# Kernel optimization log

Hardware: AMD Instinct MI355X
Metric: run time of the kernel (lower is better)

The kernel has to match this reference:

```python
import jax, jax.numpy as jnp
import numpy as np

N_NODES = 50000
N_EDGES = 600000
D = 128
BN_EPS = 1e-5


def _linear_init(key, fan_in, fan_out):
    # torch nn.Linear default: U(-1/sqrt(fan_in), 1/sqrt(fan_in)) for W and b
    kw, kb = jax.random.split(key)
    bound = 1.0 / np.sqrt(fan_in)
    W = jax.random.uniform(kw, (fan_in, fan_out), minval=-bound, maxval=bound, dtype=jnp.float32)
    b = jax.random.uniform(kb, (fan_out,), minval=-bound, maxval=bound, dtype=jnp.float32)
    return W, b


def setup_inputs() -> dict:
    key = jax.random.key(0)
    ks = jax.random.split(key, 8)
    x = jax.random.normal(ks[0], (N_NODES, D), dtype=jnp.float32)
    edge_index = jax.random.randint(ks[1], (2, N_EDGES), 0, N_NODES, dtype=jnp.int32)
    edge_attr = jax.random.normal(ks[2], (N_EDGES, D), dtype=jnp.float32)
    # MLP: [2D, D, D, D] -> Linear(2D,D)+SiLU+BN, Linear(D,D)+SiLU+BN, Linear(D,D)
    W1, b1 = _linear_init(ks[3], 2 * D, D)
    W2, b2 = _linear_init(ks[4], D, D)
    W3, b3 = _linear_init(ks[5], D, D)
    g1 = jnp.ones((D,), jnp.float32); be1 = jnp.zeros((D,), jnp.float32)
    g2 = jnp.ones((D,), jnp.float32); be2 = jnp.zeros((D,), jnp.float32)
    return {"x": x, "edge_index": edge_index, "edge_attr": edge_attr,
            "W1": W1, "b1": b1, "g1": g1, "be1": be1,
            "W2": W2, "b2": b2, "g2": g2, "be2": be2,
            "W3": W3, "b3": b3}


def _bn(h, gamma, beta):
    # BatchNorm1d in training mode: normalize with batch statistics (biased var)
    mean = jnp.mean(h, axis=0)
    var = jnp.var(h, axis=0)
    return (h - mean) * jax.lax.rsqrt(var + BN_EPS) * gamma + beta


def reference(x, edge_index, edge_attr, W1, b1, g1, be1, W2, b2, g2, be2, W3, b3):
    src = edge_index[0]
    # scatter_add over edges indexed by source node -> [N_NODES, D]
    agg = jax.ops.segment_sum(edge_attr, src, num_segments=x.shape[0])
    h = jnp.concatenate([x, agg], axis=1)  # [N, 2D]
    h = _bn(jax.nn.silu(h @ W1 + b1), g1, be1)
    h = _bn(jax.nn.silu(h @ W2 + b2), g2, be2)
    return h @ W3 + b3
```

## Files before the change

### kernel.cpp

```cpp
#include <hip/hip_runtime.h>
#include <hip/hip_bf16.h>

#define D 128

typedef __attribute__((ext_vector_type(8))) short bfrag;
typedef __attribute__((ext_vector_type(4))) float facc;
typedef __attribute__((ext_vector_type(4))) unsigned int u32x4;
typedef __attribute__((ext_vector_type(4))) float f32x4;

__device__ __forceinline__ facc mfma16(bfrag a, bfrag b, facc c) {
    return __builtin_amdgcn_mfma_f32_16x16x32_bf16(a, b, c, 0, 0, 0);
}
__device__ __forceinline__ unsigned int bf16_rn(float f) {
    unsigned int u = __float_as_uint(f);
    u += 0x7FFF + ((u >> 16) & 1);
    return u >> 16;
}
__device__ __forceinline__ float bf16_f(unsigned int h) {
    return __uint_as_float(h << 16);
}
__device__ __forceinline__ unsigned int packf(float v) {
    unsigned int hi = bf16_rn(v);
    unsigned int lo = bf16_rn(v - bf16_f(hi));
    return (hi << 16) | lo;
}

__global__ __launch_bounds__(256) void hist_kernel(
    const int* __restrict__ src, int* __restrict__ counts, int nedges) {
    int e = blockIdx.x * 256 + threadIdx.x;
    if (e < nedges) atomicAdd(&counts[src[e]], 1);
}

#define SCHUNK 2048
__global__ __launch_bounds__(256) void scanF_kernel(
    const int* __restrict__ counts, int* __restrict__ bsum,
    int* __restrict__ ctr, int* __restrict__ off, int* __restrict__ cur,
    int n, int nbk) {
    __shared__ int sd[256];
    __shared__ int sbase;
    const int tid = threadIdx.x;
    const int b = blockIdx.x;
    const int base = b * SCHUNK + tid * 8;
    int loc[8];
    int s = 0;
#pragma unroll
    for (int j = 0; j < 8; ++j) {
        int idx = base + j;
        int c = (idx < n) ? counts[idx] : 0;
        loc[j] = c;
        s += c;
    }
    sd[tid] = s;
    __syncthreads();
#pragma unroll
    for (int d2 = 1; d2 < 256; d2 <<= 1) {
        int t = (tid >= d2) ? sd[tid - d2] : 0;
        __syncthreads();
        sd[tid] += t;
        __syncthreads();
    }
    if (tid == 0) {
        atomicExch(&bsum[b], sd[255]);
        __threadfence();
        atomicAdd(ctr, 1);
        while (atomicAdd(ctr, 0) < nbk) __builtin_amdgcn_s_sleep(8);
    }
    __syncthreads();
    if (tid < 64) {
        int t = (tid < b) ? atomicAdd(&bsum[tid], 0) : 0;
#pragma unroll
        for (int o = 32; o; o >>= 1) t += __shfl_down(t, o);
        if (tid == 0) sbase = t;
    }
    __syncthreads();
    int pre = sbase + sd[tid] - s;
#pragma unroll
    for (int j = 0; j < 8; ++j) {
        int idx = base + j;
        if (idx < n) {
            off[idx] = pre;
            cur[idx] = pre;
            pre += loc[j];
        }
    }
    if (b == nbk - 1 && tid == 0) off[n] = sbase + sd[255];
}

__global__ void fill_kernel(const int* __restrict__ src, int* __restrict__ cur,
                            int* __restrict__ eid, int nedges) {
    int e = blockIdx.x * 256 + threadIdx.x;
    if (e < nedges) {
        int slot = atomicAdd(&cur[src[e]], 1);
        eid[slot] = e;
    }
}

__global__ __launch_bounds__(256) void gather_split_kernel(
    const float* __restrict__ edge_attr, const int* __restrict__ eid,
    const int* __restrict__ off, unsigned int* __restrict__ aggp, int nnodes,
    const float* __restrict__ x, unsigned int* __restrict__ xp, int n4,
    const float* __restrict__ W1, unsigned short* __restrict__ Wh,
    unsigned short* __restrict__ Wl, int gblk, int sblk) {
    const int b = blockIdx.x;
    if (b < gblk) {
        int node = b * 8 + (threadIdx.x >> 5);
        if (node >= nnodes) return;
        const int c = threadIdx.x & 31;
        int i = off[node];
        const int e = off[node + 1];
        f32x4 acc = {0.f, 0.f, 0.f, 0.f};

        for (; i + 8 <= e; i += 8) {
            int r0 = eid[i + 0], r1 = eid[i + 1], r2 = eid[i + 2],
                r3 = eid[i + 3], r4 = eid[i + 4], r5 = eid[i + 5],
                r6 = eid[i + 6], r7 = eid[i + 7];
            f32x4 v0 = __builtin_nontemporal_load(
                (const f32x4*)(edge_attr + (size_t)r0 * D) + c);
            f32x4 v1 = __builtin_nontemporal_load(
                (const f32x4*)(edge_attr + (size_t)r1 * D) + c);
            f32x4 v2 = __builtin_nontemporal_load(
                (const f32x4*)(edge_attr + (size_t)r2 * D) + c);
            f32x4 v3 = __builtin_nontemporal_load(
                (const f32x4*)(edge_attr + (size_t)r3 * D) + c);
            f32x4 v4 = __builtin_nontemporal_load(
                (const f32x4*)(edge_attr + (size_t)r4 * D) + c);
            f32x4 v5 = __builtin_nontemporal_load(
                (const f32x4*)(edge_attr + (size_t)r5 * D) + c);
            f32x4 v6 = __builtin_nontemporal_load(
                (const f32x4*)(edge_attr + (size_t)r6 * D) + c);
            f32x4 v7 = __builtin_nontemporal_load(
                (const f32x4*)(edge_attr + (size_t)r7 * D) + c);
            acc += (v0 + v1) + (v2 + v3) + ((v4 + v5) + (v6 + v7));
        }
        if (i + 4 <= e) {
            int r0 = eid[i + 0], r1 = eid[i + 1], r2 = eid[i + 2],
                r3 = eid[i + 3];
            f32x4 v0 = __builtin_nontemporal_load(
                (const f32x4*)(edge_attr + (size_t)r0 * D) + c);
            f32x4 v1 = __builtin_nontemporal_load(
                (const f32x4*)(edge_attr + (size_t)r1 * D) + c);
            f32x4 v2 = __builtin_nontemporal_load(
                (const f32x4*)(edge_attr + (size_t)r2 * D) + c);
            f32x4 v3 = __builtin_nontemporal_load(
                (const f32x4*)(edge_attr + (size_t)r3 * D) + c);
            acc += (v0 + v1) + (v2 + v3);
            i += 4;
        }
        if (i + 2 <= e) {
            int r0 = eid[i + 0], r1 = eid[i + 1];
            f32x4 v0 = __builtin_nontemporal_load(
                (const f32x4*)(edge_attr + (size_t)r0 * D) + c);
            f32x4 v1 = __builtin_nontemporal_load(
                (const f32x4*)(edge_attr + (size_t)r1 * D) + c);
            acc += v0 + v1;
            i += 2;
        }
        if (i < e) {
            acc += __builtin_nontemporal_load(
                (const f32x4*)(edge_attr + (size_t)eid[i] * D) + c);
        }
        u32x4 p;
#pragma unroll
        for (int r = 0; r < 4; ++r) p[r] = packf(acc[r]);
        *((u32x4*)(aggp + (size_t)node * D) + c) = p;
    } else if (b < gblk + sblk) {
        int i = (b - gblk) * 256 + threadIdx.x;
        if (i < n4) {
            float4 v = ((const float4*)x)[i];
            uint4 p;
            p.x = packf(v.x);
            p.y = packf(v.y);
            p.z = packf(v.z);
            p.w = packf(v.w);
            ((uint4*)xp)[i] = p;
        }
    } else {
        int j = b - gblk - sblk;
        int k = threadIdx.x;
        float w = W1[(size_t)k * D + j];
        unsigned int hi = bf16_rn(w);
        size_t o = (size_t)((k >> 3) * 128 + j) * 8 + (k & 7);
        Wh[o] = (unsigned short)hi;
        Wl[o] = (unsigned short)bf16_rn(w - bf16_f(hi));
    }
}

__global__ void fold_kernel(const float* __restrict__ sum,
                            const float* __restrict__ sq,
                            const float* __restrict__ gamma,
                            const float* __restrict__ beta,
                            const float* __restrict__ W,
                            const float* __restrict__ b,
                            unsigned short* __restrict__ Wh,
                            unsigned short* __restrict__ Wl,
                            float* __restrict__ bf, float invM) {
    int j = blockIdx.x;
    int k = threadIdx.x;
    float mean = sum[k] * invM;
    float var = sq[k] * invM - mean * mean;
    float scale = gamma[k] * rsqrtf(var + 1e-5f);
    float shift = beta[k] - mean * scale;
    float w = W[k * D + j];
    float wf = scale * w;
    unsigned int hi = bf16_rn(wf);
    size_t o = (size_t)((k >> 3) * 128 + j) * 8 + (k & 7);
    Wh[o] = (unsigned short)hi;
    Wl[o] = (unsigned short)bf16_rn(wf - bf16_f(hi));
    float v = shift * w;
#pragma unroll
    for (int of = 32; of; of >>= 1) v += __shfl_down(v, of);
    __shared__ float ws2[2];
    if ((k & 63) == 0) ws2[k >> 6] = v;
    __syncthreads();
    if (k == 0) bf[j] = b[j] + ws2[0] + ws2[1];
}

template <int K, bool SILU, bool STATS, bool PACKOUT>
__global__ __launch_bounds__(256, 2) void gemm_mfma(
    const unsigned int* __restrict__ A0, const unsigned int* __restrict__ A1,
    const unsigned short* __restrict__ Wh,
    const unsigned short* __restrict__ Wl,
    const float* __restrict__ bias, unsigned int* __restrict__ Cp,
    float* __restrict__ Cf, float* __restrict__ gsum,
    float* __restrict__ gsq, int M) {
    constexpr int NS = K / 32;
    const int tid = threadIdx.x;
    const int w = tid >> 6;
    const int l = tid & 63;
    const int lr = l & 15;
    const int lk = l >> 4;
    const int row0 = blockIdx.x * 128 + w * 32;

    facc acc[2][8];
#pragma unroll
    for (int rt = 0; rt < 2; ++rt)
#pragma unroll
        for (int ct = 0; ct < 8; ++ct)
#pragma unroll
            for (int r = 0; r < 4; ++r) acc[rt][ct][r] = 0.f;

    for (int s = 0; s < NS; ++s) {
        const int kb = s * 32 + lk * 8;
        bfrag ah[2], al[2];
#pragma unroll
        for (int rt = 0; rt < 2; ++rt) {
            const int arow = row0 + rt * 16 + lr;
            const unsigned int* As = A0;
            int kk = kb;
            if (K == 256 && s >= 4) { As = A1; kk = kb - 128; }
            u32x4 q0 = {0u, 0u, 0u, 0u}, q1 = {0u, 0u, 0u, 0u};
            if (arow < M) {
                const u32x4* p = (const u32x4*)(As + (size_t)arow * D + kk);
                q0 = p[0];
                q1 = p[1];
            }
            unsigned int ua[8] = {q0.x, q0.y, q0.z, q0.w,
                                  q1.x, q1.y, q1.z, q1.w};
            u32x4 uh, ul;
#pragma unroll
            for (int r = 0; r < 4; ++r) {
                uh[r] = __builtin_amdgcn_perm(ua[2 * r + 1], ua[2 * r],
                                              0x07060302u);
                ul[r] = __builtin_amdgcn_perm(ua[2 * r + 1], ua[2 * r],
                                              0x05040100u);
            }
            ah[rt] = __builtin_bit_cast(bfrag, uh);
            al[rt] = __builtin_bit_cast(bfrag, ul);
        }
        bfrag bh[8], bl[8];
        const int fb = (s * 4 + lk) * 128;
#pragma unroll
        for (int ct = 0; ct < 8; ++ct) {
            size_t o = (size_t)(fb + ct * 16 + lr) * 8;
            bh[ct] = *(const bfrag*)(Wh + o);
            bl[ct] = *(const bfrag*)(Wl + o);
        }
#pragma unroll
        for (int rt = 0; rt < 2; ++rt)
#pragma unroll
            for (int ct = 0; ct < 8; ++ct)
                acc[rt][ct] = mfma16(ah[rt], bh[ct], acc[rt][ct]);
#pragma unroll
        for (int rt = 0; rt < 2; ++rt)
#pragma unroll
            for (int ct = 0; ct < 8; ++ct)
                acc[rt][ct] = mfma16(ah[rt], bl[ct], acc[rt][ct]);
#pragma unroll
        for (int rt = 0; rt < 2; ++rt)
#pragma unroll
            for (int ct = 0; ct < 8; ++ct)
                acc[rt][ct] = mfma16(al[rt], bh[ct], acc[rt][ct]);
    }

    __shared__ float sred[2][4][128];
#pragma unroll
    for (int ct = 0; ct < 8; ++ct) {
        const int col = ct * 16 + lr;
        const float bj = bias[col];
        float s = 0.f, q = 0.f;
#pragma unroll
        for (int rt = 0; rt < 2; ++rt) {
            const int base = row0 + rt * 16 + lk * 4;
#pragma unroll
            for (int r = 0; r < 4; ++r) {
                int crow = base + r;
                if (crow < M) {
                    float v = acc[rt][ct][r] + bj;
                    if (SILU) v = v / (1.0f + __expf(-v));
                    if (PACKOUT) Cp[(size_t)crow * D + col] = packf(v);
                    else         Cf[(size_t)crow * D + col] = v;
                    if (STATS) { s += v; q += v * v; }
                }
            }
        }
        if (STATS) {
            s += __shfl_xor(s, 16);
            s += __shfl_xor(s, 32);
            q += __shfl_xor(q, 16);
            q += __shfl_xor(q, 32);
            if (lk == 0) {
                sred[0][w][col] = s;
                sred[1][w][col] = q;
            }
        }
    }
    if (STATS) {
        __syncthreads();
        if (tid < 128) {
            float v = sred[0][0][tid] + sred[0][1][tid] + sred[0][2][tid] +
                      sred[0][3][tid];
            unsafeAtomicAdd(&gsum[tid], v);
        } else {
            int c = tid - 128;
            float v = sred[1][0][c] + sred[1][1][c] + sred[1][2][c] +
                      sred[1][3][c];
            unsafeAtomicAdd(&gsq[c], v);
        }
    }
}

extern "C" void kernel_launch(void* const* d_in, const int* in_sizes, int n_in,
                              void* d_out, int out_size, void* d_ws,
                              size_t ws_size, hipStream_t stream) {
    const float* x     = (const float*)d_in[0];
    const int*   eidx  = (const int*)d_in[1];
    const float* eattr = (const float*)d_in[2];
    const float* W1  = (const float*)d_in[3];
    const float* b1  = (const float*)d_in[4];
    const float* g1  = (const float*)d_in[5];
    const float* be1 = (const float*)d_in[6];
    const float* W2  = (const float*)d_in[7];
    const float* b2  = (const float*)d_in[8];
    const float* g2  = (const float*)d_in[9];
    const float* be2 = (const float*)d_in[10];
    const float* W3  = (const float*)d_in[11];
    const float* b3  = (const float*)d_in[12];

    const int M = in_sizes[0] / D;
    const int E = in_sizes[1] / 2;
    const int* srcIdx = eidx;

    unsigned int* wsu = (unsigned int*)d_ws;
    unsigned int* aggp = wsu;
    unsigned int* xp   = aggp + (size_t)M * D;
    unsigned int* h1p  = xp + (size_t)M * D;
    unsigned int* h2p  = h1p + (size_t)M * D;
    int* counts = (int*)(h2p + (size_t)M * D);
    int* ctr    = counts + M;
    float* sum1 = (float*)(ctr + 4);
    float* sq1  = sum1 + D;
    float* sum2 = sq1 + D;
    float* sq2  = sum2 + D;
    float* b2f  = sq2 + D;
    float* b3f  = b2f + D;
    int* off    = (int*)(b3f + D);
    int* cur    = off + M + 4;
    int* eid    = cur + M;
    int* bsum   = eid + E;
    unsigned short* W1h = (unsigned short*)(bsum + 64);
    unsigned short* W1l = W1h + 256 * D;
    unsigned short* W2h = W1l + 256 * D;
    unsigned short* W2l = W2h + D * D;
    unsigned short* W3h = W2l + D * D;
    unsigned short* W3l = W3h + D * D;

    float* out = (float*)d_out;

    (void)hipMemsetAsync(counts, 0, ((size_t)M + 4 + 4 * D) * sizeof(int),
                         stream);

    const int eblk = (E + 255) / 256;
    hist_kernel<<<eblk, 256, 0, stream>>>(srcIdx, counts, E);

    const int nbk = (M + SCHUNK - 1) / SCHUNK;
    scanF_kernel<<<nbk, 256, 0, stream>>>(counts, bsum, ctr, off, cur, M, nbk);
    fill_kernel<<<eblk, 256, 0, stream>>>(srcIdx, cur, eid, E);

    const int gblk = (M + 7) / 8;
    const int sblk = (M * 32 + 255) / 256;
    gather_split_kernel<<<gblk + sblk + 128, 256, 0, stream>>>(
        eattr, eid, off, aggp, M, x, xp, M * 32, W1, W1h, W1l, gblk, sblk);

    int nblk = (M + 127) / 128;
    gemm_mfma<256, true, true, true><<<nblk, 256, 0, stream>>>(
        xp, aggp, W1h, W1l, b1, h1p, nullptr, sum1, sq1, M);
    fold_kernel<<<D, D, 0, stream>>>(sum1, sq1, g1, be1, W2, b2, W2h, W2l,
                                     b2f, 1.0f / (float)M);
    gemm_mfma<128, true, true, true><<<nblk, 256, 0, stream>>>(
        h1p, nullptr, W2h, W2l, b2f, h2p, nullptr, sum2, sq2, M);
    fold_kernel<<<D, D, 0, stream>>>(sum2, sq2, g2, be2, W3, b3, W3h, W3l,
                                     b3f, 1.0f / (float)M);
    gemm_mfma<128, false, false, false><<<nblk, 256, 0, stream>>>(
        h2p, nullptr, W3h, W3l, b3f, nullptr, out, nullptr, nullptr, M);
}
```

Before: 237.6 us.

## Fuse three MLP GEMMs and BN folds into one persistent kernel with grid barriers

Replaces the three GEMM launches and two fold launches with a single kernel that keeps each block's 128-row activation tile in LDS across layers. Global atomic counters serve as grid-wide barriers so BN statistics and the folded weights are complete before the next layer starts. This removes the h1/h2 round-trips through global memory and four kernel launches. The cost is a large LDS footprint that may lower occupancy, and the spin barriers need all 391 blocks to be resident at once, which risks deadlock or serialization if they are not.

```diff
diff --git a/kernel.cpp b/kernel.cpp
--- a/kernel.cpp
+++ b/kernel.cpp
@@ -23,6 +23,17 @@
     unsigned int hi = bf16_rn(v);
     unsigned int lo = bf16_rn(v - bf16_f(hi));
     return (hi << 16) | lo;
+}
+__device__ __forceinline__ void splitA(const unsigned int ua[8], bfrag& ah,
+                                       bfrag& al) {
+    u32x4 uh, ul;
+#pragma unroll
+    for (int r = 0; r < 4; ++r) {
+        uh[r] = __builtin_amdgcn_perm(ua[2 * r + 1], ua[2 * r], 0x07060302u);
+        ul[r] = __builtin_amdgcn_perm(ua[2 * r + 1], ua[2 * r], 0x05040100u);
+    }
+    ah = __builtin_bit_cast(bfrag, uh);
+    al = __builtin_bit_cast(bfrag, ul);
 }
 
 __global__ __launch_bounds__(256) void hist_kernel(
@@ -185,52 +196,40 @@
     }
 }
 
-__global__ void fold_kernel(const float* __restrict__ sum,
-                            const float* __restrict__ sq,
-                            const float* __restrict__ gamma,
-                            const float* __restrict__ beta,
-                            const float* __restrict__ W,
-                            const float* __restrict__ b,
-                            unsigned short* __restrict__ Wh,
-                            unsigned short* __restrict__ Wl,
-                            float* __restrict__ bf, float invM) {
-    int j = blockIdx.x;
-    int k = threadIdx.x;
-    float mean = sum[k] * invM;
-    float var = sq[k] * invM - mean * mean;
-    float scale = gamma[k] * rsqrtf(var + 1e-5f);
-    float shift = beta[k] - mean * scale;
-    float w = W[k * D + j];
-    float wf = scale * w;
-    unsigned int hi = bf16_rn(wf);
-    size_t o = (size_t)((k >> 3) * 128 + j) * 8 + (k & 7);
-    Wh[o] = (unsigned short)hi;
-    Wl[o] = (unsigned short)bf16_rn(wf - bf16_f(hi));
-    float v = shift * w;
-#pragma unroll
-    for (int of = 32; of; of >>= 1) v += __shfl_down(v, of);
-    __shared__ float ws2[2];
-    if ((k & 63) == 0) ws2[k >> 6] = v;
-    __syncthreads();
-    if (k == 0) bf[j] = b[j] + ws2[0] + ws2[1];
-}
-
-template <int K, bool SILU, bool STATS, bool PACKOUT>
-__global__ __launch_bounds__(256, 2) void gemm_mfma(
-    const unsigned int* __restrict__ A0, const unsigned int* __restrict__ A1,
+__device__ __forceinline__ void fold_inkernel(
+    float (&sred)[2][4][128], float* gsum, float* gsq,
+    const float* __restrict__ gamma, const float* __restrict__ beta,
+    const float* __restrict__ W, const float* __restrict__ b,
+    unsigned short* __restrict__ Wh, unsigned short* __restrict__ Wl,
+    float* __restrict__ bf, float invM, int tid, int j) {
+    if (tid < 128) {
+        int k = tid;
+        float mean = unsafeAtomicAdd(&gsum[k], 0.0f) * invM;
+        float var = unsafeAtomicAdd(&gsq[k], 0.0f) * invM - mean * mean;
+        float scale = gamma[k] * rsqrtf(var + 1e-5f);
+        float shift = beta[k] - mean * scale;
+        float wv = W[k * D + j];
+        float wf = scale * wv;
+        unsigned int hi = bf16_rn(wf);
+        size_t o = (size_t)((k >> 3) * 128 + j) * 8 + (k & 7);
+        Wh[o] = (unsigned short)hi;
+        Wl[o] = (unsigned short)bf16_rn(wf - bf16_f(hi));
+        float v = shift * wv;
+#pragma unroll
+        for (int of = 32; of; of >>= 1) v += __shfl_down(v, of);
+        if ((k & 63) == 0) sred[0][0][k >> 6] = v;
+    }
+    __syncthreads();
+    if (tid == 0) bf[j] = b[j] + sred[0][0][0] + sred[0][0][1];
+}
+
+template <bool SILU, bool STATS, bool TO_LDS>
+__device__ __forceinline__ void lds_gemm_phase(
+    unsigned int (&hs)[128][132], float (&sred)[2][4][128],
     const unsigned short* __restrict__ Wh,
-    const unsigned short* __restrict__ Wl,
-    const float* __restrict__ bias, unsigned int* __restrict__ Cp,
-    float* __restrict__ Cf, float* __restrict__ gsum,
-    float* __restrict__ gsq, int M) {
-    constexpr int NS = K / 32;
-    const int tid = threadIdx.x;
-    const int w = tid >> 6;
-    const int l = tid & 63;
-    const int lr = l & 15;
-    const int lk = l >> 4;
-    const int row0 = blockIdx.x * 128 + w * 32;
-
+    const unsigned short* __restrict__ Wl, const float* __restrict__ bias,
+    float* gsum, float* gsq, float* __restrict__ outp, int tid, int w, int lr,
+    int lk, int row0g, int M) {
     facc acc[2][8];
 #pragma unroll
     for (int rt = 0; rt < 2; ++rt)
@@ -239,33 +238,17 @@
 #pragma unroll
             for (int r = 0; r < 4; ++r) acc[rt][ct][r] = 0.f;
 
-    for (int s = 0; s < NS; ++s) {
+    for (int s = 0; s < 4; ++s) {
         const int kb = s * 32 + lk * 8;
         bfrag ah[2], al[2];
 #pragma unroll
         for (int rt = 0; rt < 2; ++rt) {
-            const int arow = row0 + rt * 16 + lr;
-            const unsigned int* As = A0;
-            int kk = kb;
-            if (K == 256 && s >= 4) { As = A1; kk = kb - 128; }
-            u32x4 q0 = {0u, 0u, 0u, 0u}, q1 = {0u, 0u, 0u, 0u};
-            if (arow < M) {
-                const u32x4* p = (const u32x4*)(As + (size_t)arow * D + kk);
-                q0 = p[0];
-                q1 = p[1];
-            }
+            const int lrow = w * 32 + rt * 16 + lr;
+            const u32x4* p = (const u32x4*)&hs[lrow][kb];
+            u32x4 q0 = p[0], q1 = p[1];
             unsigned int ua[8] = {q0.x, q0.y, q0.z, q0.w,
                                   q1.x, q1.y, q1.z, q1.w};
-            u32x4 uh, ul;
-#pragma unroll
-            for (int r = 0; r < 4; ++r) {
-                uh[r] = __builtin_amdgcn_perm(ua[2 * r + 1], ua[2 * r],
-                                              0x07060302u);
-                ul[r] = __builtin_amdgcn_perm(ua[2 * r + 1], ua[2 * r],
-                                              0x05040100u);
-            }
-            ah[rt] = __builtin_bit_cast(bfrag, uh);
-            al[rt] = __builtin_bit_cast(bfrag, ul);
+            splitA(ua, ah[rt], al[rt]);
         }
         bfrag bh[8], bl[8];
         const int fb = (s * 4 + lk) * 128;
@@ -292,35 +275,38 @@
                 acc[rt][ct] = mfma16(al[rt], bh[ct], acc[rt][ct]);
     }
 
-    __shared__ float sred[2][4][128];
 #pragma unroll
     for (int ct = 0; ct < 8; ++ct) {
         const int col = ct * 16 + lr;
         const float bj = bias[col];
-        float s = 0.f, q = 0.f;
+        float s_ = 0.f, q_ = 0.f;
 #pragma unroll
         for (int rt = 0; rt < 2; ++rt) {
-            const int base = row0 + rt * 16 + lk * 4;
+            const int lbase = w * 32 + rt * 16 + lk * 4;
 #pragma unroll
             for (int r = 0; r < 4; ++r) {
-                int crow = base + r;
-                if (crow < M) {
-                    float v = acc[rt][ct][r] + bj;
-                    if (SILU) v = v / (1.0f + __expf(-v));
-                    if (PACKOUT) Cp[(size_t)crow * D + col] = packf(v);
-                    else         Cf[(size_t)crow * D + col] = v;
-                    if (STATS) { s += v; q += v * v; }
+                float v = acc[rt][ct][r] + bj;
+                if (SILU) v = v / (1.0f + __expf(-v));
+                int crow = row0g + lbase + r;
+                if (TO_LDS) {
+                    hs[lbase + r][col] = packf(v);
+                } else {
+                    if (crow < M) outp[(size_t)crow * D + col] = v;
+                }
+                if (STATS && crow < M) {
+                    s_ += v;
+                    q_ += v * v;
                 }
             }
         }
         if (STATS) {
-            s += __shfl_xor(s, 16);
-            s += __shfl_xor(s, 32);
-            q += __shfl_xor(q, 16);
-            q += __shfl_xor(q, 32);
+            s_ += __shfl_xor(s_, 16);
+            s_ += __shfl_xor(s_, 32);
+            q_ += __shfl_xor(q_, 16);
+            q_ += __shfl_xor(q_, 32);
             if (lk == 0) {
-                sred[0][w][col] = s;
-                sred[1][w][col] = q;
+                sred[0][w][col] = s_;
+                sred[1][w][col] = q_;
             }
         }
     }
@@ -337,6 +323,170 @@
             unsafeAtomicAdd(&gsq[c], v);
         }
     }
+}
+
+__global__ __launch_bounds__(256, 2) void mlp_fused(
+    const unsigned int* __restrict__ xp, const unsigned int* __restrict__ aggp,
+    const unsigned short* __restrict__ W1h,
+    const unsigned short* __restrict__ W1l, const float* __restrict__ b1,
+    const float* __restrict__ g1, const float* __restrict__ be1,
+    const float* __restrict__ W2, const float* __restrict__ b2,
+    const float* __restrict__ g2, const float* __restrict__ be2,
+    const float* __restrict__ W3, const float* __restrict__ b3,
+    unsigned short* __restrict__ W2h, unsigned short* __restrict__ W2l,
+    float* __restrict__ b2f, unsigned short* __restrict__ W3h,
+    unsigned short* __restrict__ W3l, float* __restrict__ b3f,
+    float* sum1, float* sq1, float* sum2, float* sq2, int* ctrs,
+    float* __restrict__ out, int M, float invM) {
+    __shared__ unsigned int hs[128][132];
+    __shared__ float sred[2][4][128];
+    const int tid = threadIdx.x;
+    const int w = tid >> 6;
+    const int l = tid & 63;
+    const int lr = l & 15;
+    const int lk = l >> 4;
+    const int row0g = blockIdx.x * 128;
+    const int nblk = (int)gridDim.x;
+
+    {
+        facc acc[2][8];
+#pragma unroll
+        for (int rt = 0; rt < 2; ++rt)
+#pragma unroll
+            for (int ct = 0; ct < 8; ++ct)
+#pragma unroll
+                for (int r = 0; r < 4; ++r) acc[rt][ct][r] = 0.f;
+
+        for (int s = 0; s < 8; ++s) {
+            const int kb = s * 32 + lk * 8;
+            bfrag ah[2], al[2];
+#pragma unroll
+            for (int rt = 0; rt < 2; ++rt) {
+                const int arow = row0g + w * 32 + rt * 16 + lr;
+                const unsigned int* As = (s < 4) ? xp : aggp;
+                const int kk = (s < 4) ? kb : kb - 128;
+                u32x4 q0 = {0u, 0u, 0u, 0u}, q1 = {0u, 0u, 0u, 0u};
+                if (arow < M) {
+                    const u32x4* p =
+                        (const u32x4*)(As + (size_t)arow * D + kk);
+                    q0 = p[0];
+                    q1 = p[1];
+                }
+                unsigned int ua[8] = {q0.x, q0.y, q0.z, q0.w,
+                                      q1.x, q1.y, q1.z, q1.w};
+                splitA(ua, ah[rt], al[rt]);
+            }
+            bfrag bh[8], bl[8];
+            const int fb = (s * 4 + lk) * 128;
+#pragma unroll
+            for (int ct = 0; ct < 8; ++ct) {
+                size_t o = (size_t)(fb + ct * 16 + lr) * 8;
+                bh[ct] = *(const bfrag*)(W1h + o);
+                bl[ct] = *(const bfrag*)(W1l + o);
+            }
+#pragma unroll
+            for (int rt = 0; rt < 2; ++rt)
+#pragma unroll
+                for (int ct = 0; ct < 8; ++ct)
+                    acc[rt][ct] = mfma16(ah[rt], bh[ct], acc[rt][ct]);
+#pragma unroll
+            for (int rt = 0; rt < 2; ++rt)
+#pragma unroll
+                for (int ct = 0; ct < 8; ++ct)
+                    acc[rt][ct] = mfma16(ah[rt], bl[ct], acc[rt][ct]);
+#pragma unroll
+            for (int rt = 0; rt < 2; ++rt)
+#pragma unroll
+                for (int ct = 0; ct < 8; ++ct)
+                    acc[rt][ct] = mfma16(al[rt], bh[ct], acc[rt][ct]);
+        }
+#pragma unroll
+        for (int ct = 0; ct < 8; ++ct) {
+            const int col = ct * 16 + lr;
+            const float bj = b1[col];
+            float s_ = 0.f, q_ = 0.f;
+#pragma unroll
+            for (int rt = 0; rt < 2; ++rt) {
+                const int lbase = w * 32 + rt * 16 + lk * 4;
+#pragma unroll
+                for (int r = 0; r < 4; ++r) {
+                    float v = acc[rt][ct][r] + bj;
+                    v = v / (1.0f + __expf(-v));
+                    hs[lbase + r][col] = packf(v);
+                    if (row0g + lbase + r < M) {
+                        s_ += v;
+                        q_ += v * v;
+                    }
+                }
+            }
+            s_ += __shfl_xor(s_, 16);
+            s_ += __shfl_xor(s_, 32);
+            q_ += __shfl_xor(q_, 16);
+            q_ += __shfl_xor(q_, 32);
+            if (lk == 0) {
+                sred[0][w][col] = s_;
+                sred[1][w][col] = q_;
+            }
+        }
+        __syncthreads();
+        if (tid < 128) {
+            float v = sred[0][0][tid] + sred[0][1][tid] + sred[0][2][tid] +
+                      sred[0][3][tid];
+            unsafeAtomicAdd(&sum1[tid], v);
+        } else {
+            int c = tid - 128;
+            float v = sred[1][0][c] + sred[1][1][c] + sred[1][2][c] +
+                      sred[1][3][c];
+            unsafeAtomicAdd(&sq1[c], v);
+        }
+    }
+    __threadfence();
+    __syncthreads();
+    if (tid == 0) atomicAdd(&ctrs[0], 1);
+
+    if (blockIdx.x < 128) {
+        if (tid == 0)
+            while (atomicAdd(&ctrs[0], 0) < nblk) __builtin_amdgcn_s_sleep(8);
+        __syncthreads();
+        __threadfence();
+        fold_inkernel(sred, sum1, sq1, g1, be1, W2, b2, W2h, W2l, b2f, invM,
+                      tid, blockIdx.x);
+        if (tid == 0) {
+            __threadfence();
+            atomicAdd(&ctrs[1], 1);
+        }
+    }
+    if (tid == 0)
+        while (atomicAdd(&ctrs[1], 0) < 128) __builtin_amdgcn_s_sleep(8);
+    __syncthreads();
+    __threadfence();
+
+    lds_gemm_phase<true, true, true>(hs, sred, W2h, W2l, b2f, sum2, sq2,
+                                     nullptr, tid, w, lr, lk, row0g, M);
+    __threadfence();
+    __syncthreads();
+    if (tid == 0) atomicAdd(&ctrs[2], 1);
+
+    if (blockIdx.x < 128) {
+        if (tid == 0)
+            while (atomicAdd(&ctrs[2], 0) < nblk) __builtin_amdgcn_s_sleep(8);
+        __syncthreads();
+        __threadfence();
+        fold_inkernel(sred, sum2, sq2, g2, be2, W3, b3, W3h, W3l, b3f, invM,
+                      tid, blockIdx.x);
+        if (tid == 0) {
+            __threadfence();
+            atomicAdd(&ctrs[3], 1);
+        }
+    }
+    if (tid == 0)
+        while (atomicAdd(&ctrs[3], 0) < 128) __builtin_amdgcn_s_sleep(8);
+    __syncthreads();
+    __threadfence();
+
+    lds_gemm_phase<false, false, false>(hs, sred, W3h, W3l, b3f, nullptr,
+                                        nullptr, out, tid, w, lr, lk, row0g,
+                                        M);
 }
 
 extern "C" void kernel_launch(void* const* d_in, const int* in_sizes, int n_in,
@@ -363,11 +513,9 @@
     unsigned int* wsu = (unsigned int*)d_ws;
     unsigned int* aggp = wsu;
     unsigned int* xp   = aggp + (size_t)M * D;
-    unsigned int* h1p  = xp + (size_t)M * D;
-    unsigned int* h2p  = h1p + (size_t)M * D;
-    int* counts = (int*)(h2p + (size_t)M * D);
-    int* ctr    = counts + M;
-    float* sum1 = (float*)(ctr + 4);
+    int* counts = (int*)(xp + (size_t)M * D);
+    int* ctrs   = counts + M;
+    float* sum1 = (float*)(ctrs + 8);
     float* sq1  = sum1 + D;
     float* sum2 = sq1 + D;
     float* sq2  = sum2 + D;
@@ -386,14 +534,15 @@
 
     float* out = (float*)d_out;
 
-    (void)hipMemsetAsync(counts, 0, ((size_t)M + 4 + 4 * D) * sizeof(int),
+    (void)hipMemsetAsync(counts, 0, ((size_t)M + 8 + 4 * D) * sizeof(int),
                          stream);
 
     const int eblk = (E + 255) / 256;
     hist_kernel<<<eblk, 256, 0, stream>>>(srcIdx, counts, E);
 
     const int nbk = (M + SCHUNK - 1) / SCHUNK;
-    scanF_kernel<<<nbk, 256, 0, stream>>>(counts, bsum, ctr, off, cur, M, nbk);
+    scanF_kernel<<<nbk, 256, 0, stream>>>(counts, bsum, &ctrs[4], off, cur, M,
+                                          nbk);
     fill_kernel<<<eblk, 256, 0, stream>>>(srcIdx, cur, eid, E);
 
     const int gblk = (M + 7) / 8;
@@ -401,15 +550,9 @@
     gather_split_kernel<<<gblk + sblk + 128, 256, 0, stream>>>(
         eattr, eid, off, aggp, M, x, xp, M * 32, W1, W1h, W1l, gblk, sblk);
 
-    int nblk = (M + 127) / 128;
-    gemm_mfma<256, true, true, true><<<nblk, 256, 0, stream>>>(
-        xp, aggp, W1h, W1l, b1, h1p, nullptr, sum1, sq1, M);
-    fold_kernel<<<D, D, 0, stream>>>(sum1, sq1, g1, be1, W2, b2, W2h, W2l,
-                                     b2f, 1.0f / (float)M);
-    gemm_mfma<128, true, true, true><<<nblk, 256, 0, stream>>>(
-        h1p, nullptr, W2h, W2l, b2f, h2p, nullptr, sum2, sq2, M);
-    fold_kernel<<<D, D, 0, stream>>>(sum2, sq2, g2, be2, W3, b3, W3h, W3l,
-                                     b3f, 1.0f / (float)M);
-    gemm_mfma<128, false, false, false><<<nblk, 256, 0, stream>>>(
-        h2p, nullptr, W3h, W3l, b3f, nullptr, out, nullptr, nullptr, M);
-}
+    const int nblk = (M + 127) / 128;
+    mlp_fused<<<nblk, 256, 0, stream>>>(
+        xp, aggp, W1h, W1l, b1, g1, be1, W2, b2, g2, be2, W3, b3, W2h, W2l,
+        b2f, W3h, W3l, b3f, sum1, sq1, sum2, sq2, ctrs, out, M,
+        1.0f / (float)M);
+}
```

Measured after the change: 366.7 us. 54.4% more time.
